# Kernel tuning notes

Measured on AMD Instinct MI355X. Metric: run time of the kernel, lower is better.

Reference implementation:

```python
import jax, jax.numpy as jnp
import numpy as np

FREQ_DIM = 32
TIME_DIM = 32
HEADS = 8
TWO_PI = 6.283185307179586


def get_embeddings(B, H, W, freq_dim, time_dim, dtype):
    # freq embeddings over the height (frequency) axis
    nf = freq_dim // 2
    ln_x = jnp.log2(jnp.arange(0, H * nf, dtype=jnp.float32))
    ln_x = ln_x.at[0].set(-2.0)
    ln_x = ln_x.reshape(H, nf).T  # [nf, H]
    ln_x = ln_x * jnp.arange(1, nf + 1, dtype=jnp.float32)[:, None]
    # view_as_real(exp(1j*theta)) -> (cos, sin), interleaved per order along channel dim
    freq = jnp.stack([jnp.cos(ln_x), jnp.sin(ln_x)], axis=1).reshape(freq_dim, H)  # [freq_dim, H]
    freq = jnp.broadcast_to(freq[None, :, :, None], (B, freq_dim, H, W))

    # time embeddings over the width (time) axis
    nt = time_dim // 2
    k = jnp.arange(0, nt, dtype=jnp.float32) + 0.5  # [nt]
    x = jnp.arange(0, nt * W, dtype=jnp.float32).reshape(W, nt).T  # [nt, W]
    theta = k[:, None] * x / (W * nt) * TWO_PI  # [nt, W]
    time = jnp.stack([jnp.cos(theta), jnp.sin(theta)], axis=1).reshape(time_dim, W)  # [time_dim, W]
    time = jnp.broadcast_to(time[None, :, None, :], (B, time_dim, H, W))

    return jnp.concatenate([freq, time], axis=1).astype(dtype)  # [B, freq_dim+time_dim, H, W]


def setup_inputs() -> dict:
    key = jax.random.key(0)
    ks = jax.random.split(key, 6)
    B, C, H, W = 2, 512, 64, 32
    qkC = C + FREQ_DIM + TIME_DIM  # 576
    inner = HEADS * 64  # 512
    return {
        "hidden_states": jax.random.normal(ks[0], (B, C, H, W), dtype=jnp.float32),
        "Wq": jax.random.normal(ks[1], (qkC, inner), dtype=jnp.float32) * 0.02,
        "Wk": jax.random.normal(ks[2], (qkC, inner), dtype=jnp.float32) * 0.02,
        "Wv": jax.random.normal(ks[3], (C, inner), dtype=jnp.float32) * 0.02,
        "Wout": jax.random.normal(ks[4], (inner, C), dtype=jnp.float32) * 0.02,
        "bout": jnp.zeros((C,), dtype=jnp.float32),
    }


def reference(hidden_states, Wq, Wk, Wv, Wout, bout):
    B, C, H, W = hidden_states.shape
    emb = get_embeddings(B, H, W, FREQ_DIM, TIME_DIM, hidden_states.dtype)
    qk_hs = jnp.concatenate([hidden_states, emb], axis=1)  # [B, qkC, H, W]

    S = H * W
    qk_hs = qk_hs.reshape(B, -1, S).transpose(0, 2, 1)  # [B, S, qkC]
    v_hs = hidden_states.reshape(B, C, S).transpose(0, 2, 1)  # [B, S, C]

    q = qk_hs @ Wq  # [B, S, inner]
    k = qk_hs @ Wk
    v = v_hs @ Wv

    hd_qk = q.shape[-1] // HEADS
    hd_v = v.shape[-1] // HEADS
    q = q.reshape(B, S, HEADS, hd_qk).transpose(0, 2, 1, 3)  # [B, h, S, d]
    k = k.reshape(B, S, HEADS, hd_qk).transpose(0, 2, 1, 3)
    v = v.reshape(B, S, HEADS, hd_v).transpose(0, 2, 1, 3)

    scale = 1.0 / jnp.sqrt(jnp.asarray(hd_qk, dtype=q.dtype))
    scores = jnp.einsum('bhqd,bhkd->bhqk', q, k) * scale
    attn = jax.nn.softmax(scores, axis=-1)
    o = jnp.einsum('bhqk,bhkd->bhqd', attn, v)  # [B, h, S, d_v]

    o = o.transpose(0, 2, 1, 3).reshape(B, S, HEADS * hd_v)
    o = o @ Wout + bout  # [B, S, C]
    o = o.transpose(0, 2, 1).reshape(B, C, H, W)

    return o + hidden_states  # residual_connection=True, rescale_output_factor=1.0
```

## Files before the change

### kernel.cpp

```cpp
#include <hip/hip_runtime.h>
#include <math.h>

#define B_    2
#define C_    512
#define H_    64
#define W_    32
#define S_    2048
#define QKC_  576
#define INNER_ 512
#define NH_   8
#define HD_   64
#define TWO_PI_ 6.283185307179586f

typedef __attribute__((ext_vector_type(8))) short bfrag;
typedef __attribute__((ext_vector_type(4))) float ffrag;
typedef __attribute__((ext_vector_type(16))) float f16v;

typedef __attribute__((address_space(1))) const unsigned int as1_u32;
typedef __attribute__((address_space(3))) unsigned int as3_u32;

__device__ __forceinline__ ushort f2bf(float f) {
    unsigned u = __builtin_bit_cast(unsigned, f);
    unsigned r = (u + 0x7FFFu + ((u >> 16) & 1u)) >> 16;
    return (ushort)r;
}

__device__ __forceinline__ f16v zero16() {
    f16v z;
    #pragma unroll
    for (int i = 0; i < 16; i++) z[i] = 0.f;
    return z;
}

#define GLD(gp_, lp_) __builtin_amdgcn_global_load_lds((as1_u32*)(gp_), (as3_u32*)(lp_), 16, 0, 0)
#define EXPA(dst_, x_) asm("v_exp_f32 %0, %1" : "=v"(dst_) : "v"(x_))
#define SC_LOG2E 0.18033688011f

__global__ void k_trans_emb(const float* __restrict__ hid, ushort* __restrict__ X) {
    __shared__ float t[32][33];
    int b  = blockIdx.z;
    int s0 = blockIdx.x * 32, c0 = blockIdx.y * 32;
    int tx = threadIdx.x, ty = threadIdx.y;
    if (c0 < 512) {
        t[ty][tx] = hid[((size_t)b * C_ + (c0 + ty)) * S_ + s0 + tx];
        __syncthreads();
        X[((size_t)(b * S_ + s0 + ty)) * QKC_ + c0 + tx] = f2bf(t[tx][ty]);
    } else {
        int c = c0 - 512 + tx;
        int s = s0 + ty;
        int h = s >> 5, w = s & 31;
        float val;
        if (c < 32) {
            int f = c >> 1;
            int n = h * 16 + f;
            float lx = (n == 0) ? -2.0f : log2f((float)n);
            float arg = lx * (float)(f + 1);
            val = (c & 1) ? sinf(arg) : cosf(arg);
        } else {
            int tt = (c - 32) >> 1;
            float theta = ((float)tt + 0.5f) * (float)(w * 16 + tt) * (TWO_PI_ / 512.0f);
            val = (c & 1) ? sinf(theta) : cosf(theta);
        }
        X[(size_t)(b * S_ + s) * QKC_ + c0 + tx] = f2bf(val);
    }
}

__global__ void k_wtrans_all(const float* __restrict__ Wq, const float* __restrict__ Wk,
                             const float* __restrict__ Wv, const float* __restrict__ Wo,
                             ushort* __restrict__ Wqt, ushort* __restrict__ Wkt,
                             ushort* __restrict__ Wvt, ushort* __restrict__ Wot) {
    __shared__ float t[32][33];
    int z = blockIdx.z;
    const float* W; ushort* Wt; int K;
    if (z == 0)      { W = Wq; Wt = Wqt; K = QKC_; }
    else if (z == 1) { W = Wk; Wt = Wkt; K = QKC_; }
    else if (z == 2) { W = Wv; Wt = Wvt; K = C_; }
    else             { W = Wo; Wt = Wot; K = INNER_; }
    int k0 = blockIdx.x * 32, n0 = blockIdx.y * 32;
    if (k0 >= K) return;
    int tx = threadIdx.x, ty = threadIdx.y;
    t[ty][tx] = W[(size_t)(k0 + ty) * 512 + n0 + tx];
    __syncthreads();
    Wt[(size_t)(n0 + ty) * K + k0 + tx] = f2bf(t[tx][ty]);
}

#define GSTAGE(buf_, k0_) {                                                   \
    _Pragma("unroll")                                                         \
    for (int i_ = 0; i_ < 6; i_++)                                            \
        GLD(gp[i_] + (k0_), tl + (buf_) * 12288 + lo[i_]); }

__global__ __launch_bounds__(256, 3) void k_qkv(const ushort* __restrict__ X,
                                                const ushort* __restrict__ Wqt,
                                                const ushort* __restrict__ Wkt,
                                                const ushort* __restrict__ Wvt,
                                                ushort* __restrict__ Qb,
                                                ushort* __restrict__ Kbb,
                                                ushort* __restrict__ Vtg) {
    __shared__ ushort __attribute__((aligned(16))) tl[2 * 12288];

    int tid = threadIdx.x;
    int l = tid & 63, wv = tid >> 6;
    int wr = wv >> 1, wc = wv & 1;
    int bid = blockIdx.x;
    int lgc = (bid & 7) * 96 + (bid >> 3);
    int bx = lgc % 24, by = lgc / 24;
    int n0 = bx * 64, m0 = by * 128;
    int sel = n0 >> 9, n0l = n0 & 511;
    const ushort* Bt = (sel == 0) ? Wqt : (sel == 1) ? Wkt : Wvt;
    const int K = (sel < 2) ? QKC_ : C_;
    const int nst = K >> 6;
    int l15 = l & 15, lg = l >> 4;
    int swz = l15 & 7;

    const ushort* gp[6];
    unsigned lo[6];
    {
        int rsub = l >> 3;
        int clog = (l & 7) ^ rsub;
        #pragma unroll
        for (int i = 0; i < 6; i++) {
            int c = wv * 6 + i;
            lo[i] = c * 512;
            if (c < 16) gp[i] = X  + (size_t)(m0  + c * 8        + rsub) * QKC_ + clog * 8;
            else        gp[i] = Bt + (size_t)(n0l + (c - 16) * 8 + rsub) * K    + clog * 8;
        }
    }

    ffrag acc[4][2];
    #pragma unroll
    for (int i = 0; i < 4; i++)
        #pragma unroll
        for (int j = 0; j < 2; j++) acc[i][j] = (ffrag){0.f, 0.f, 0.f, 0.f};

    GSTAGE(0, 0);
    int cur = 0;
    for (int kt = 0; kt < nst; kt++) {
        __syncthreads();
        if (kt + 1 < nst) GSTAGE(cur ^ 1, (kt + 1) * 64);
        const ushort* As = tl + cur * 12288;
        const ushort* Bs = As + 8192;
        #pragma unroll
        for (int ks = 0; ks < 2; ks++) {
            int cl = ks * 4 + lg;
            int ch = (cl ^ swz) * 8;
            bfrag af[4], bf[2];
            #pragma unroll
            for (int mi = 0; mi < 4; mi++)
                af[mi] = *(const bfrag*)(As + (wr * 64 + mi * 16 + l15) * 64 + ch);
            #pragma unroll
            for (int nj = 0; nj < 2; nj++)
                bf[nj] = *(const bfrag*)(Bs + (wc * 32 + nj * 16 + l15) * 64 + ch);
            #pragma unroll
            for (int mi = 0; mi < 4; mi++)
                #pragma unroll
                for (int nj = 0; nj < 2; nj++)
                    acc[mi][nj] = __builtin_amdgcn_mfma_f32_16x16x32_bf16(af[mi], bf[nj], acc[mi][nj], 0, 0, 0);
        }
        cur ^= 1;
    }

    if (sel < 2) {
        ushort* Co = sel ? Kbb : Qb;
        #pragma unroll
        for (int mi = 0; mi < 4; mi++)
            #pragma unroll
            for (int nj = 0; nj < 2; nj++)
                #pragma unroll
                for (int r = 0; r < 4; r++) {
                    int row = m0 + wr * 64 + mi * 16 + lg * 4 + r;
                    int col = n0l + wc * 32 + nj * 16 + l15;
                    Co[(size_t)row * INNER_ + col] = f2bf(acc[mi][nj][r]);
                }
    } else {
        ushort (*Ct)[136] = (ushort(*)[136])tl;
        __syncthreads();
        #pragma unroll
        for (int mi = 0; mi < 4; mi++)
            #pragma unroll
            for (int nj = 0; nj < 2; nj++)
                #pragma unroll
                for (int r = 0; r < 4; r++)
                    Ct[wc * 32 + nj * 16 + l15][wr * 64 + mi * 16 + lg * 4 + r] = f2bf(acc[mi][nj][r]);
        __syncthreads();
        int b = m0 >> 11, s0m = m0 & 2047;
        #pragma unroll
        for (int p = 0; p < 4; p++) {
            int c = tid + p * 256;
            int rowc = c >> 4, mc = c & 15;
            uint4 v = *(uint4*)&Ct[rowc][mc * 8];
            *(uint4*)(Vtg + (((size_t)(b * 512 + n0l + rowc)) << 11) + s0m + mc * 8) = v;
        }
    }
}

__global__ __launch_bounds__(256, 2) void k_og(const ushort* __restrict__ Ob,
                                               const ushort* __restrict__ Wot,
                                               const float* __restrict__ bias,
                                               const float* __restrict__ hid,
                                               float* __restrict__ out) {
    __shared__ ushort __attribute__((aligned(16))) tl[2 * 12288];

    int tid = threadIdx.x;
    int l = tid & 63, wv = tid >> 6;
    int wr = wv >> 1, wc = wv & 1;
    int bid = blockIdx.x;
    int lgc = (bid & 7) * 32 + (bid >> 3);
    int bx = lgc & 7, by = lgc >> 3;
    int n0 = bx * 64, m0 = by * 128;
    int l15 = l & 15, lg = l >> 4;
    int swz = l15 & 7;

    const ushort* gp[6];
    unsigned lo[6];
    {
        int rsub = l >> 3;
        int clog = (l & 7) ^ rsub;
        #pragma unroll
        for (int i = 0; i < 6; i++) {
            int c = wv * 6 + i;
            lo[i] = c * 512;
            if (c < 16) gp[i] = Ob  + (size_t)(m0 + c * 8        + rsub) * INNER_ + clog * 8;
            else        gp[i] = Wot + (size_t)(n0 + (c - 16) * 8 + rsub) * INNER_ + clog * 8;
        }
    }

    ffrag acc[4][2];
    #pragma unroll
    for (int i = 0; i < 4; i++)
        #pragma unroll
        for (int j = 0; j < 2; j++) acc[i][j] = (ffrag){0.f, 0.f, 0.f, 0.f};

    GSTAGE(0, 0);
    int cur = 0;
    for (int kt = 0; kt < 8; kt++) {
        __syncthreads();
        if (kt < 7) GSTAGE(cur ^ 1, (kt + 1) * 64);
        const ushort* As = tl + cur * 12288;
        const ushort* Bs = As + 8192;
        #pragma unroll
        for (int ks = 0; ks < 2; ks++) {
            int cl = ks * 4 + lg;
            int ch = (cl ^ swz) * 8;
            bfrag af[4], bf[2];
            #pragma unroll
            for (int mi = 0; mi < 4; mi++)
                af[mi] = *(const bfrag*)(As + (wr * 64 + mi * 16 + l15) * 64 + ch);
            #pragma unroll
            for (int nj = 0; nj < 2; nj++)
                bf[nj] = *(const bfrag*)(Bs + (wc * 32 + nj * 16 + l15) * 64 + ch);
            #pragma unroll
            for (int mi = 0; mi < 4; mi++)
                #pragma unroll
                for (int nj = 0; nj < 2; nj++)
                    acc[mi][nj] = __builtin_amdgcn_mfma_f32_16x16x32_bf16(af[mi], bf[nj], acc[mi][nj], 0, 0, 0);
        }
        cur ^= 1;
    }

    float (*Cf)[129] = (float(*)[129])tl;
    float bv[2];
    #pragma unroll
    for (int nj = 0; nj < 2; nj++) bv[nj] = bias[n0 + wc * 32 + nj * 16 + l15];
    __syncthreads();
    #pragma unroll
    for (int mi = 0; mi < 4; mi++)
        #pragma unroll
        for (int nj = 0; nj < 2; nj++)
            #pragma unroll
            for (int r = 0; r < 4; r++)
                Cf[wc * 32 + nj * 16 + l15][wr * 64 + mi * 16 + lg * 4 + r] = acc[mi][nj][r] + bv[nj];
    __syncthreads();
    int b = m0 >> 11, s0m = m0 & 2047;
    #pragma unroll
    for (int p = 0; p < 8; p++) {
        int f = p * 256 + tid;
        int c = f >> 5, sq = (f & 31) * 4;
        size_t o = (((size_t)(b * 512 + n0 + c)) << 11) + s0m + sq;
        float4 hv = *(const float4*)(hid + o);
        float4 cv = *(float4*)&Cf[c][sq];
        cv.x += hv.x; cv.y += hv.y; cv.z += hv.z; cv.w += hv.w;
        *(float4*)(out + o) = cv;
    }
}

#define CVTPK(dst, a, b) asm("v_cvt_pk_bf16_f32 %0, %1, %2" : "=v"(dst) : "v"(a), "v"(b))
#define SWAP32(a, b)     asm("v_permlane32_swap_b32 %0, %1" : "+v"(a), "+v"(b))

#define STAGE(buf_, kt_) {                                                    \
    const ushort* g_ = gsrc + (size_t)(kt_) * ktstride;                       \
    ushort* lp_ = ktv + (buf_) * 16384 + wv * 4096;                           \
    _Pragma("unroll")                                                         \
    for (int i_ = 0; i_ < 8; i_++)                                            \
        GLD(g_ + (size_t)i_ * istride, lp_ + i_ * 512); }

__global__ __launch_bounds__(256, 2) void k_attn(const ushort* __restrict__ Qf,
                                                 const ushort* __restrict__ Kf,
                                                 const ushort* __restrict__ Vtg,
                                                 ushort* __restrict__ Ob) {
    __shared__ ushort __attribute__((aligned(16))) ktv[2 * 4 * 4096];
    __shared__ float mlsh[2][2][2][32];

    const int id = blockIdx.x;
    const int lgc = (id & 7) * 64 + (id >> 3);
    const int qb = lgc & 31;
    const int hb = lgc >> 5;
    const int hd = hb & 7, b = hb >> 3;

    const int tid = threadIdx.x;
    const int l = tid & 63, wv = tid >> 6;
    const int wp = wv >> 1, hh = wv & 1;
    const int l31 = l & 31, hi = l >> 5, swz = l31 & 7;
    const int hoff = hd * HD_;
    const int brow = b * S_ + qb * 64;

    bfrag qf[4];
    {
        const ushort* qp = Qf + (size_t)(brow + wp * 32 + l31) * INNER_ + hoff + hi * 8;
        #pragma unroll
        for (int ks = 0; ks < 4; ks++) qf[ks] = *(const bfrag*)(qp + ks * 16);
    }

    const int hv = wv >> 1, isV = wv & 1;
    const int rr = l >> 3;
    const int clog = (l & 7) ^ rr;
    const ushort* gsrc;
    size_t istride, ktstride;
    if (isV) {
        gsrc = Vtg + (size_t)(b * 512 + hoff + rr) * 2048 + hv * 1024 + clog * 8;
        istride = (size_t)8 * 2048;
        ktstride = 64;
    } else {
        gsrc = Kf + (size_t)(b * S_ + hv * 1024 + rr) * INNER_ + hoff + clog * 8;
        istride = (size_t)8 * INNER_;
        ktstride = (size_t)64 * INNER_;
    }

    STAGE(0, 0);

    float m_run = -INFINITY, l_run = 0.f;
    f16v acc0 = zero16(), acc1 = zero16();
    int cur = 0;

    for (int kt = 0; kt < 16; kt++) {
        __syncthreads();
        if (kt < 15) STAGE(cur ^ 1, kt + 1);

        const ushort* Kt  = ktv + cur * 16384 + hh * 8192;
        const ushort* Vtt = Kt + 4096;

        f16v sf0 = zero16(), sf1 = zero16();
        __builtin_amdgcn_s_setprio(1);
        #pragma unroll
        for (int ks = 0; ks < 4; ks++) {
            int ch = ((ks * 2 + hi) ^ swz) * 8;
            bfrag k0 = *(const bfrag*)(Kt + l31 * 64 + ch);
            bfrag k1 = *(const bfrag*)(Kt + (l31 + 32) * 64 + ch);
            sf0 = __builtin_amdgcn_mfma_f32_32x32x16_bf16(k0, qf[ks], sf0, 0, 0, 0);
            sf1 = __builtin_amdgcn_mfma_f32_32x32x16_bf16(k1, qf[ks], sf1, 0, 0, 0);
        }
        __builtin_amdgcn_s_setprio(0);

        float tm = -INFINITY;
        #pragma unroll
        for (int j = 0; j < 16; j++) { tm = fmaxf(tm, sf0[j]); tm = fmaxf(tm, sf1[j]); }
        tm = fmaxf(tm, __shfl_xor(tm, 32));
        if (!__all(tm <= m_run + 64.0f)) {
            float mn = fmaxf(m_run, tm);
            float corr; EXPA(corr, (m_run - mn) * SC_LOG2E);
            l_run *= corr;
            #pragma unroll
            for (int j = 0; j < 16; j++) { acc0[j] *= corr; acc1[j] *= corr; }
            m_run = mn;
        }
        float nm = -m_run * SC_LOG2E;
        float ls = 0.f;
        #pragma unroll
        for (int j = 0; j < 16; j++) { float p; EXPA(p, fmaf(sf0[j], SC_LOG2E, nm)); sf0[j] = p; ls += p; }
        #pragma unroll
        for (int j = 0; j < 16; j++) { float p; EXPA(p, fmaf(sf1[j], SC_LOG2E, nm)); sf1[j] = p; ls += p; }
        ls += __shfl_xor(ls, 32);
        l_run += ls;

        __builtin_amdgcn_s_setprio(1);
        #pragma unroll
        for (int s = 0; s < 2; s++) {
            unsigned A0, B0, A1, B1;
            CVTPK(A0, sf0[s * 8 + 0], sf0[s * 8 + 1]); CVTPK(B0, sf0[s * 8 + 4], sf0[s * 8 + 5]);
            SWAP32(A0, B0);
            CVTPK(A1, sf0[s * 8 + 2], sf0[s * 8 + 3]); CVTPK(B1, sf0[s * 8 + 6], sf0[s * 8 + 7]);
            SWAP32(A1, B1);
            uint4 u; u.x = A0; u.y = A1; u.z = B0; u.w = B1;
            bfrag pa = __builtin_bit_cast(bfrag, u);
            int ch = ((s * 2 + hi) ^ swz) * 8;
            bfrag v0 = *(const bfrag*)(Vtt + l31 * 64 + ch);
            bfrag v1 = *(const bfrag*)(Vtt + (l31 + 32) * 64 + ch);
            acc0 = __builtin_amdgcn_mfma_f32_32x32x16_bf16(v0, pa, acc0, 0, 0, 0);
            acc1 = __builtin_amdgcn_mfma_f32_32x32x16_bf16(v1, pa, acc1, 0, 0, 0);
        }
        #pragma unroll
        for (int s = 0; s < 2; s++) {
            unsigned A0, B0, A1, B1;
            CVTPK(A0, sf1[s * 8 + 0], sf1[s * 8 + 1]); CVTPK(B0, sf1[s * 8 + 4], sf1[s * 8 + 5]);
            SWAP32(A0, B0);
            CVTPK(A1, sf1[s * 8 + 2], sf1[s * 8 + 3]); CVTPK(B1, sf1[s * 8 + 6], sf1[s * 8 + 7]);
            SWAP32(A1, B1);
            uint4 u; u.x = A0; u.y = A1; u.z = B0; u.w = B1;
            bfrag pa = __builtin_bit_cast(bfrag, u);
            int ch = (((2 + s) * 2 + hi) ^ swz) * 8;
            bfrag v0 = *(const bfrag*)(Vtt + l31 * 64 + ch);
            bfrag v1 = *(const bfrag*)(Vtt + (l31 + 32) * 64 + ch);
            acc0 = __builtin_amdgcn_mfma_f32_32x32x16_bf16(v0, pa, acc0, 0, 0, 0);
            acc1 = __builtin_amdgcn_mfma_f32_32x32x16_bf16(v1, pa, acc1, 0, 0, 0);
        }
        __builtin_amdgcn_s_setprio(0);

        cur ^= 1;
    }

    if (l < 32) { mlsh[wp][hh][0][l] = m_run; mlsh[wp][hh][1][l] = l_run; }
    __syncthreads();
    float mo  = mlsh[wp][hh ^ 1][0][l31];
    float lo_ = mlsh[wp][hh ^ 1][1][l31];
    float mn2 = fmaxf(m_run, mo);
    float cs, co;
    EXPA(cs, (m_run - mn2) * SC_LOG2E);
    EXPA(co, (mo    - mn2) * SC_LOG2E);
    float inv = 1.0f / (cs * l_run + co * lo_);

    float* cmb = (float*)ktv;
    if (hh == 0) {
        #pragma unroll
        for (int j = 0; j < 16; j++) {
            int d0 = (j & 3) + 8 * (j >> 2) + 4 * hi;
            cmb[wp * 2112 + d0 * 33 + l31]        = cs * acc0[j];
            cmb[wp * 2112 + (d0 + 32) * 33 + l31] = cs * acc1[j];
        }
    }
    __syncthreads();
    if (hh == 1) {
        #pragma unroll
        for (int j = 0; j < 16; j++) {
            int d0 = (j & 3) + 8 * (j >> 2) + 4 * hi;
            int i0 = wp * 2112 + d0 * 33 + l31;
            int i1 = wp * 2112 + (d0 + 32) * 33 + l31;
            cmb[i0] = (cmb[i0] + cs * acc0[j]) * inv;
            cmb[i1] = (cmb[i1] + cs * acc1[j]) * inv;
        }
    }
    __syncthreads();
    #pragma unroll
    for (int p2 = 0; p2 < 2; p2++) {
        int f = p2 * 256 + tid;
        int q = f >> 3, dc = f & 7;
        int wpp = q >> 5, ql = q & 31;
        bfrag ov;
        #pragma unroll
        for (int j2 = 0; j2 < 8; j2++)
            ov[j2] = (short)f2bf(cmb[wpp * 2112 + (dc * 8 + j2) * 33 + ql]);
        *(uint4*)(Ob + (size_t)(brow + q) * INNER_ + hoff + dc * 8) = __builtin_bit_cast(uint4, ov);
    }
}

extern "C" void kernel_launch(void* const* d_in, const int* in_sizes, int n_in,
                              void* d_out, int out_size, void* d_ws, size_t ws_size,
                              hipStream_t stream) {
    const float* hid  = (const float*)d_in[0];
    const float* Wq   = (const float*)d_in[1];
    const float* Wk   = (const float*)d_in[2];
    const float* Wv   = (const float*)d_in[3];
    const float* Wout = (const float*)d_in[4];
    const float* bout = (const float*)d_in[5];
    float* out = (float*)d_out;

    const int M = B_ * S_;
    char* w = (char*)d_ws;
    ushort* X    = (ushort*)w;                    w += (size_t)M * QKC_ * 2;
    ushort* Qb   = (ushort*)w;                    w += (size_t)M * INNER_ * 2;
    ushort* Kbb  = (ushort*)w;                    w += (size_t)M * INNER_ * 2;
    ushort* Vtg  = (ushort*)w;                    w += (size_t)M * INNER_ * 2;
    ushort* Ob   = (ushort*)w;                    w += (size_t)M * INNER_ * 2;
    ushort* Wqt  = (ushort*)w;                    w += (size_t)INNER_ * QKC_ * 2;
    ushort* Wkt  = (ushort*)w;                    w += (size_t)INNER_ * QKC_ * 2;
    ushort* Wvt  = (ushort*)w;                    w += (size_t)INNER_ * C_ * 2;
    ushort* Wot  = (ushort*)w;                    w += (size_t)C_ * INNER_ * 2;

    k_wtrans_all<<<dim3(18, 16, 4), dim3(32, 32), 0, stream>>>(Wq, Wk, Wv, Wout,
                                                               Wqt, Wkt, Wvt, Wot);
    k_trans_emb<<<dim3(S_ / 32, 18, B_), dim3(32, 32), 0, stream>>>(hid, X);

    k_qkv<<<dim3(768), 256, 0, stream>>>(X, Wqt, Wkt, Wvt, Qb, Kbb, Vtg);

    k_attn<<<dim3(512), 256, 0, stream>>>(Qb, Kbb, Vtg, Ob);

    k_og<<<dim3(256), 256, 0, stream>>>(Ob, Wot, bout, hid, out);
}
```

Baseline: 65.92 us.

## Pre-pack K/V into MFMA fragment layout and split attention KV across four waves

The QKV GEMM now writes K and V in a packed, fragment-ready layout per (batch, head) pair, so the attention kernel can stage tiles with contiguous loads and read fragments without swizzle math. The attention kernel grows to 512 threads, with each wave handling a quarter of the key sequence for a 32-query group instead of two halves. Partial results are combined across four splits in shared memory. This raises parallelism per block and simplifies the loads, at the cost of more shared memory (about 68KB), a heavier cross-wave reduction, and a more complex epilogue in the QKV kernel.

```diff
diff --git a/kernel.cpp b/kernel.cpp
--- a/kernel.cpp
+++ b/kernel.cpp
@@ -94,8 +94,8 @@
                                                 const ushort* __restrict__ Wkt,
                                                 const ushort* __restrict__ Wvt,
                                                 ushort* __restrict__ Qb,
-                                                ushort* __restrict__ Kbb,
-                                                ushort* __restrict__ Vtg) {
+                                                ushort* __restrict__ Kpk,
+                                                ushort* __restrict__ Vpk) {
     __shared__ ushort __attribute__((aligned(16))) tl[2 * 12288];
 
     int tid = threadIdx.x;
@@ -159,8 +159,7 @@
         cur ^= 1;
     }
 
-    if (sel < 2) {
-        ushort* Co = sel ? Kbb : Qb;
+    if (sel == 0) {
         #pragma unroll
         for (int mi = 0; mi < 4; mi++)
             #pragma unroll
@@ -169,7 +168,7 @@
                 for (int r = 0; r < 4; r++) {
                     int row = m0 + wr * 64 + mi * 16 + lg * 4 + r;
                     int col = n0l + wc * 32 + nj * 16 + l15;
-                    Co[(size_t)row * INNER_ + col] = f2bf(acc[mi][nj][r]);
+                    Qb[(size_t)row * INNER_ + col] = f2bf(acc[mi][nj][r]);
                 }
     } else {
         ushort (*Ct)[136] = (ushort(*)[136])tl;
@@ -182,13 +181,28 @@
                 for (int r = 0; r < 4; r++)
                     Ct[wc * 32 + nj * 16 + l15][wr * 64 + mi * 16 + lg * 4 + r] = f2bf(acc[mi][nj][r]);
         __syncthreads();
-        int b = m0 >> 11, s0m = m0 & 2047;
-        #pragma unroll
-        for (int p = 0; p < 4; p++) {
-            int c = tid + p * 256;
-            int rowc = c >> 4, mc = c & 15;
-            uint4 v = *(uint4*)&Ct[rowc][mc * 8];
-            *(uint4*)(Vtg + (((size_t)(b * 512 + n0l + rowc)) << 11) + s0m + mc * 8) = v;
+        int pair = (m0 >> 11) * 8 + (n0l >> 6);
+        int kvb0 = (m0 & 2047) >> 5;
+        if (sel == 1) {
+            #pragma unroll
+            for (int p = 0; p < 4; p++) {
+                int cid = tid + p * 256;
+                int sl = cid >> 7, kv = cid & 127;
+                bfrag tmp;
+                #pragma unroll
+                for (int j = 0; j < 8; j++) tmp[j] = (short)Ct[sl * 8 + j][kv];
+                ushort* dst = Kpk + ((size_t)((pair * 64 + kvb0 + (kv >> 5)) * 8 + sl)) * 256 + (kv & 31) * 8;
+                *(uint4*)dst = __builtin_bit_cast(uint4, tmp);
+            }
+        } else {
+            #pragma unroll
+            for (int p = 0; p < 4; p++) {
+                int cid = tid + p * 256;
+                int d = cid >> 4, mc = cid & 15;
+                uint4 v = *(uint4*)&Ct[d][mc * 8];
+                ushort* dst = Vpk + ((size_t)((pair * 64 + kvb0 + (mc >> 2)) * 4 + (mc & 3))) * 512 + d * 8;
+                *(uint4*)dst = v;
+            }
         }
     }
 }
@@ -286,83 +300,73 @@
 #define CVTPK(dst, a, b) asm("v_cvt_pk_bf16_f32 %0, %1, %2" : "=v"(dst) : "v"(a), "v"(b))
 #define SWAP32(a, b)     asm("v_permlane32_swap_b32 %0, %1" : "+v"(a), "+v"(b))
 
-#define STAGE(buf_, kt_) {                                                    \
-    const ushort* g_ = gsrc + (size_t)(kt_) * ktstride;                       \
-    ushort* lp_ = ktv + (buf_) * 16384 + wv * 4096;                           \
+#define ASTAGE(buf_, kt_) {                                                   \
+    const ushort* g_ = (qg ? vpb : kpb) + (size_t)(kt_) * 2048 + l * 8;       \
+    ushort* lp_ = ktv + spb + (buf_) * 4096 + (qg ? 2048 : 0);                \
     _Pragma("unroll")                                                         \
-    for (int i_ = 0; i_ < 8; i_++)                                            \
-        GLD(g_ + (size_t)i_ * istride, lp_ + i_ * 512); }
-
-__global__ __launch_bounds__(256, 2) void k_attn(const ushort* __restrict__ Qf,
-                                                 const ushort* __restrict__ Kf,
-                                                 const ushort* __restrict__ Vtg,
+    for (int i_ = 0; i_ < 4; i_++)                                            \
+        GLD(g_ + i_ * 512, lp_ + i_ * 512); }
+
+__global__ __launch_bounds__(512, 4) void k_attn(const ushort* __restrict__ Qf,
+                                                 const ushort* __restrict__ Kpk,
+                                                 const ushort* __restrict__ Vpk,
                                                  ushort* __restrict__ Ob) {
-    __shared__ ushort __attribute__((aligned(16))) ktv[2 * 4 * 4096];
-    __shared__ float mlsh[2][2][2][32];
+    __shared__ __attribute__((aligned(16))) char smem[69632];
+    ushort* ktv = (ushort*)smem;
+    float*  cmb = (float*)smem;
+    float*  mlsh = (float*)(smem + 67584);
 
     const int id = blockIdx.x;
     const int lgc = (id & 7) * 64 + (id >> 3);
-    const int qb = lgc & 31;
-    const int hb = lgc >> 5;
-    const int hd = hb & 7, b = hb >> 3;
+    const int qb = lgc & 31, pair = lgc >> 5;
+    const int hd = pair & 7, b = pair >> 3;
 
     const int tid = threadIdx.x;
     const int l = tid & 63, wv = tid >> 6;
-    const int wp = wv >> 1, hh = wv & 1;
-    const int l31 = l & 31, hi = l >> 5, swz = l31 & 7;
+    const int qg = wv >> 2, sp = wv & 3;
+    const int l31 = l & 31, hi = l >> 5;
     const int hoff = hd * HD_;
     const int brow = b * S_ + qb * 64;
 
     bfrag qf[4];
     {
-        const ushort* qp = Qf + (size_t)(brow + wp * 32 + l31) * INNER_ + hoff + hi * 8;
+        const ushort* qp = Qf + (size_t)(brow + qg * 32 + l31) * INNER_ + hoff + hi * 8;
         #pragma unroll
         for (int ks = 0; ks < 4; ks++) qf[ks] = *(const bfrag*)(qp + ks * 16);
     }
 
-    const int hv = wv >> 1, isV = wv & 1;
-    const int rr = l >> 3;
-    const int clog = (l & 7) ^ rr;
-    const ushort* gsrc;
-    size_t istride, ktstride;
-    if (isV) {
-        gsrc = Vtg + (size_t)(b * 512 + hoff + rr) * 2048 + hv * 1024 + clog * 8;
-        istride = (size_t)8 * 2048;
-        ktstride = 64;
-    } else {
-        gsrc = Kf + (size_t)(b * S_ + hv * 1024 + rr) * INNER_ + hoff + clog * 8;
-        istride = (size_t)8 * INNER_;
-        ktstride = (size_t)64 * INNER_;
-    }
-
-    STAGE(0, 0);
+    const ushort* kpb = Kpk + ((size_t)pair * 64 + sp * 16) * 2048;
+    const ushort* vpb = Vpk + ((size_t)pair * 64 + sp * 16) * 2048;
+    const int spb  = sp * 8192;
+    const int koff = l31 * 8 + hi * 256;
+    const int voff = l31 * 8 + hi * 512;
+
+    ASTAGE(0, 0);
 
     float m_run = -INFINITY, l_run = 0.f;
     f16v acc0 = zero16(), acc1 = zero16();
-    int cur = 0;
+    int buf = 0;
 
     for (int kt = 0; kt < 16; kt++) {
         __syncthreads();
-        if (kt < 15) STAGE(cur ^ 1, kt + 1);
-
-        const ushort* Kt  = ktv + cur * 16384 + hh * 8192;
-        const ushort* Vtt = Kt + 4096;
-
-        f16v sf0 = zero16(), sf1 = zero16();
-        __builtin_amdgcn_s_setprio(1);
+        if (kt < 15) ASTAGE(buf ^ 1, kt + 1);
+
+        const ushort* Kt = ktv + spb + buf * 4096;
+        const ushort* Vt = Kt + 2048;
+
+        f16v sf0 = zero16();
         #pragma unroll
         for (int ks = 0; ks < 4; ks++) {
-            int ch = ((ks * 2 + hi) ^ swz) * 8;
-            bfrag k0 = *(const bfrag*)(Kt + l31 * 64 + ch);
-            bfrag k1 = *(const bfrag*)(Kt + (l31 + 32) * 64 + ch);
-            sf0 = __builtin_amdgcn_mfma_f32_32x32x16_bf16(k0, qf[ks], sf0, 0, 0, 0);
-            sf1 = __builtin_amdgcn_mfma_f32_32x32x16_bf16(k1, qf[ks], sf1, 0, 0, 0);
-        }
-        __builtin_amdgcn_s_setprio(0);
-
-        float tm = -INFINITY;
-        #pragma unroll
-        for (int j = 0; j < 16; j++) { tm = fmaxf(tm, sf0[j]); tm = fmaxf(tm, sf1[j]); }
+            bfrag kfr = *(const bfrag*)(Kt + ks * 512 + koff);
+            sf0 = __builtin_amdgcn_mfma_f32_32x32x16_bf16(kfr, qf[ks], sf0, 0, 0, 0);
+        }
+
+        float t8[8];
+        #pragma unroll
+        for (int j = 0; j < 8; j++) t8[j] = fmaxf(sf0[j], sf0[j + 8]);
+        float t4a = fmaxf(t8[0], t8[4]), t4b = fmaxf(t8[1], t8[5]);
+        float t4c = fmaxf(t8[2], t8[6]), t4d = fmaxf(t8[3], t8[7]);
+        float tm = fmaxf(fmaxf(t4a, t4b), fmaxf(t4c, t4d));
         tm = fmaxf(tm, __shfl_xor(tm, 32));
         if (!__all(tm <= m_run + 64.0f)) {
             float mn = fmaxf(m_run, tm);
@@ -373,15 +377,15 @@
             m_run = mn;
         }
         float nm = -m_run * SC_LOG2E;
-        float ls = 0.f;
-        #pragma unroll
-        for (int j = 0; j < 16; j++) { float p; EXPA(p, fmaf(sf0[j], SC_LOG2E, nm)); sf0[j] = p; ls += p; }
-        #pragma unroll
-        for (int j = 0; j < 16; j++) { float p; EXPA(p, fmaf(sf1[j], SC_LOG2E, nm)); sf1[j] = p; ls += p; }
+        #pragma unroll
+        for (int j = 0; j < 16; j++) { float p; EXPA(p, fmaf(sf0[j], SC_LOG2E, nm)); sf0[j] = p; }
+        float s8[8];
+        #pragma unroll
+        for (int j = 0; j < 8; j++) s8[j] = sf0[j] + sf0[j + 8];
+        float ls = ((s8[0] + s8[4]) + (s8[1] + s8[5])) + ((s8[2] + s8[6]) + (s8[3] + s8[7]));
         ls += __shfl_xor(ls, 32);
         l_run += ls;
 
-        __builtin_amdgcn_s_setprio(1);
         #pragma unroll
         for (int s = 0; s < 2; s++) {
             unsigned A0, B0, A1, B1;
@@ -391,73 +395,56 @@
             SWAP32(A1, B1);
             uint4 u; u.x = A0; u.y = A1; u.z = B0; u.w = B1;
             bfrag pa = __builtin_bit_cast(bfrag, u);
-            int ch = ((s * 2 + hi) ^ swz) * 8;
-            bfrag v0 = *(const bfrag*)(Vtt + l31 * 64 + ch);
-            bfrag v1 = *(const bfrag*)(Vtt + (l31 + 32) * 64 + ch);
+            bfrag v0 = *(const bfrag*)(Vt + s * 1024 + voff);
+            bfrag v1 = *(const bfrag*)(Vt + s * 1024 + voff + 256);
             acc0 = __builtin_amdgcn_mfma_f32_32x32x16_bf16(v0, pa, acc0, 0, 0, 0);
             acc1 = __builtin_amdgcn_mfma_f32_32x32x16_bf16(v1, pa, acc1, 0, 0, 0);
         }
-        #pragma unroll
-        for (int s = 0; s < 2; s++) {
-            unsigned A0, B0, A1, B1;
-            CVTPK(A0, sf1[s * 8 + 0], sf1[s * 8 + 1]); CVTPK(B0, sf1[s * 8 + 4], sf1[s * 8 + 5]);
-            SWAP32(A0, B0);
-            CVTPK(A1, sf1[s * 8 + 2], sf1[s * 8 + 3]); CVTPK(B1, sf1[s * 8 + 6], sf1[s * 8 + 7]);
-            SWAP32(A1, B1);
-            uint4 u; u.x = A0; u.y = A1; u.z = B0; u.w = B1;
-            bfrag pa = __builtin_bit_cast(bfrag, u);
-            int ch = (((2 + s) * 2 + hi) ^ swz) * 8;
-            bfrag v0 = *(const bfrag*)(Vtt + l31 * 64 + ch);
-            bfrag v1 = *(const bfrag*)(Vtt + (l31 + 32) * 64 + ch);
-            acc0 = __builtin_amdgcn_mfma_f32_32x32x16_bf16(v0, pa, acc0, 0, 0, 0);
-            acc1 = __builtin_amdgcn_mfma_f32_32x32x16_bf16(v1, pa, acc1, 0, 0, 0);
-        }
-        __builtin_amdgcn_s_setprio(0);
-
-        cur ^= 1;
-    }
-
-    if (l < 32) { mlsh[wp][hh][0][l] = m_run; mlsh[wp][hh][1][l] = l_run; }
+
+        buf ^= 1;
+    }
+
+    if (hi == 0) {
+        mlsh[(qg * 4 + sp) * 64 + l31]      = m_run;
+        mlsh[(qg * 4 + sp) * 64 + 32 + l31] = l_run;
+    }
     __syncthreads();
-    float mo  = mlsh[wp][hh ^ 1][0][l31];
-    float lo_ = mlsh[wp][hh ^ 1][1][l31];
-    float mn2 = fmaxf(m_run, mo);
-    float cs, co;
-    EXPA(cs, (m_run - mn2) * SC_LOG2E);
-    EXPA(co, (mo    - mn2) * SC_LOG2E);
-    float inv = 1.0f / (cs * l_run + co * lo_);
-
-    float* cmb = (float*)ktv;
-    if (hh == 0) {
+    {
+        float* creg = cmb + (qg * 4 + sp) * 2112;
         #pragma unroll
         for (int j = 0; j < 16; j++) {
             int d0 = (j & 3) + 8 * (j >> 2) + 4 * hi;
-            cmb[wp * 2112 + d0 * 33 + l31]        = cs * acc0[j];
-            cmb[wp * 2112 + (d0 + 32) * 33 + l31] = cs * acc1[j];
+            creg[d0 * 33 + l31]        = acc0[j];
+            creg[(d0 + 32) * 33 + l31] = acc1[j];
         }
     }
     __syncthreads();
-    if (hh == 1) {
-        #pragma unroll
-        for (int j = 0; j < 16; j++) {
-            int d0 = (j & 3) + 8 * (j >> 2) + 4 * hi;
-            int i0 = wp * 2112 + d0 * 33 + l31;
-            int i1 = wp * 2112 + (d0 + 32) * 33 + l31;
-            cmb[i0] = (cmb[i0] + cs * acc0[j]) * inv;
-            cmb[i1] = (cmb[i1] + cs * acc1[j]) * inv;
-        }
-    }
-    __syncthreads();
-    #pragma unroll
-    for (int p2 = 0; p2 < 2; p2++) {
-        int f = p2 * 256 + tid;
-        int q = f >> 3, dc = f & 7;
-        int wpp = q >> 5, ql = q & 31;
+    {
+        int qgE = tid >> 8;
+        int t2 = tid & 255;
+        int qq = t2 >> 3, cc = t2 & 7;
+        float mh[4], lh[4], cs[4];
+        float mg = -INFINITY;
+        #pragma unroll
+        for (int h = 0; h < 4; h++) {
+            mh[h] = mlsh[(qgE * 4 + h) * 64 + qq];
+            lh[h] = mlsh[(qgE * 4 + h) * 64 + 32 + qq];
+            mg = fmaxf(mg, mh[h]);
+        }
+        float tot = 0.f;
+        #pragma unroll
+        for (int h = 0; h < 4; h++) { EXPA(cs[h], (mh[h] - mg) * SC_LOG2E); tot += cs[h] * lh[h]; }
+        float inv = 1.0f / tot;
         bfrag ov;
         #pragma unroll
-        for (int j2 = 0; j2 < 8; j2++)
-            ov[j2] = (short)f2bf(cmb[wpp * 2112 + (dc * 8 + j2) * 33 + ql]);
-        *(uint4*)(Ob + (size_t)(brow + q) * INNER_ + hoff + dc * 8) = __builtin_bit_cast(uint4, ov);
+        for (int j = 0; j < 8; j++) {
+            int d = cc * 8 + j;
+            float s = 0.f;
+            #pragma unroll
+            for (int h = 0; h < 4; h++) s += cs[h] * cmb[(qgE * 4 + h) * 2112 + d * 33 + qq];
+            ov[j] = (short)f2bf(s * inv);
+        }
+        *(uint4*)(Ob + (size_t)(brow + qgE * 32 + qq) * INNER_ + hoff + cc * 8) = __builtin_bit_cast(uint4, ov);
     }
 }
 
@@ -476,8 +463,8 @@
     char* w = (char*)d_ws;
     ushort* X    = (ushort*)w;                    w += (size_t)M * QKC_ * 2;
     ushort* Qb   = (ushort*)w;                    w += (size_t)M * INNER_ * 2;
-    ushort* Kbb  = (ushort*)w;                    w += (size_t)M * INNER_ * 2;
-    ushort* Vtg  = (ushort*)w;                    w += (size_t)M * INNER_ * 2;
+    ushort* Kpk  = (ushort*)w;                    w += (size_t)M * INNER_ * 2;
+    ushort* Vpk  = (ushort*)w;                    w += (size_t)M * INNER_ * 2;
     ushort* Ob   = (ushort*)w;                    w += (size_t)M * INNER_ * 2;
     ushort* Wqt  = (ushort*)w;                    w += (size_t)INNER_ * QKC_ * 2;
     ushort* Wkt  = (ushort*)w;                    w += (size_t)INNER_ * QKC_ * 2;
@@ -488,9 +475,9 @@
                                                                Wqt, Wkt, Wvt, Wot);
     k_trans_emb<<<dim3(S_ / 32, 18, B_), dim3(32, 32), 0, stream>>>(hid, X);
 
-    k_qkv<<<dim3(768), 256, 0, stream>>>(X, Wqt, Wkt, Wvt, Qb, Kbb, Vtg);
-
-    k_attn<<<dim3(512), 256, 0, stream>>>(Qb, Kbb, Vtg, Ob);
+    k_qkv<<<dim3(768), 256, 0, stream>>>(X, Wqt, Wkt, Wvt, Qb, Kpk, Vpk);
+
+    k_attn<<<dim3(512), 512, 0, stream>>>(Qb, Kpk, Vpk, Ob);
 
     k_og<<<dim3(256), 256, 0, stream>>>(Ob, Wot, bout, hid, out);
 }
```

Measured after the change: 66.80 us. About the same (+1.3%).
